# Optimization experiments

Hardware: AMD Instinct MI355X
Metric: run time of the kernel (lower is better)

The kernel has to match this reference:

```python
import jax, jax.numpy as jnp
import numpy as np

N, D, H1, H2, C, K = 8192, 512, 1024, 512, 10, 64
EPS_BN = 1e-5  # torch BatchNorm1d default eps


def _bn(x, g, b):
    # BatchNorm1d in training mode: per-batch stats, biased variance
    mu = x.mean(axis=0)
    var = x.var(axis=0)
    return (x - mu) / jnp.sqrt(var + EPS_BN) * g + b


def _features(x, ibn_g, ibn_b, W1, b1, g1, bb1, W2, b2, g2, bb2):
    x = _bn(x, ibn_g, ibn_b)                    # input_norm
    h = _bn(jnp.tanh(x @ W1.T + b1), g1, bb1)   # layer 1: Linear -> Tanh -> BN
    h = _bn(jnp.tanh(h @ W2.T + b2), g2, bb2)   # layer 2
    return h                                    # [N, H2]


def _nona_self(fx, fn, y_ohe):
    # sim = -cdist(fx, fn); self-neighbor path (x == x_n): -inf diag + top-k mask
    sq_x = jnp.sum(fx * fx, axis=1)
    sq_n = jnp.sum(fn * fn, axis=1)
    d2 = jnp.maximum(sq_x[:, None] + sq_n[None, :] - 2.0 * (fx @ fn.T), 0.0)
    safe = d2 > 1e-9
    dist = jnp.where(safe, jnp.sqrt(jnp.where(safe, d2, 1.0)), 0.0)
    sim = -dist
    eye = jnp.eye(N, dtype=bool)
    sim = jnp.where(eye, -jnp.inf, sim)         # sim -= inf * I
    _, idx = jax.lax.top_k(sim, K)              # [N, K]
    keep = jnp.zeros((N, N), dtype=bool).at[jnp.arange(N)[:, None], idx].set(True)
    sim = jnp.where(keep, sim, -jnp.inf)        # KNNMask: non-topk -> -inf
    probs = jax.nn.softmax(sim, axis=1)
    return jnp.clip(probs @ y_ohe, 0.0, 1.0)


def setup_inputs() -> dict:
    key = jax.random.key(0)
    ks = jax.random.split(key, 6)
    x = jax.random.normal(ks[0], (N, D), dtype=jnp.float32)
    x_n = x + 0.0  # NONA self-neighbor mode requires x_n == x elementwise
    y_n = jax.random.randint(ks[1], (N,), 0, C, dtype=jnp.int32)
    s1 = 1.0 / np.sqrt(D)
    s2 = 1.0 / np.sqrt(H1)
    W1 = jax.random.uniform(ks[2], (H1, D), jnp.float32, -s1, s1)
    b1 = jax.random.uniform(ks[3], (H1,), jnp.float32, -s1, s1)
    W2 = jax.random.uniform(ks[4], (H2, H1), jnp.float32, -s2, s2)
    b2 = jax.random.uniform(ks[5], (H2,), jnp.float32, -s2, s2)
    return {
        "x": x, "x_n": x_n, "y_n": y_n,
        "ibn_g": jnp.ones((D,), jnp.float32), "ibn_b": jnp.zeros((D,), jnp.float32),
        "W1": W1, "b1": b1, "g1": jnp.ones((H1,), jnp.float32), "bb1": jnp.zeros((H1,), jnp.float32),
        "W2": W2, "b2": b2, "g2": jnp.ones((H2,), jnp.float32), "bb2": jnp.zeros((H2,), jnp.float32),
    }


def reference(x, x_n, y_n, ibn_g, ibn_b, W1, b1, g1, bb1, W2, b2, g2, bb2):
    fx = _features(x, ibn_g, ibn_b, W1, b1, g1, bb1, W2, b2, g2, bb2)
    fn = _features(x_n, ibn_g, ibn_b, W1, b1, g1, bb1, W2, b2, g2, bb2)
    y_ohe = jax.nn.one_hot(y_n, C, dtype=jnp.float32)
    return _nona_self(fx, fn, y_ohe)
```

## Files before the change

kernel.cpp:

```cpp
#include <hip/hip_runtime.h>
#include <math.h>

#define NROWS 8192
#define DIM   512
#define HID1  1024
#define HID2  512
#define NCLS  10
#define KTOP  64
#define KPACK 1024
#define KFULL 1536
#define EPSBAND 0.02f

typedef __attribute__((ext_vector_type(8))) short short8;
typedef __attribute__((ext_vector_type(4))) float f32x4;

__device__ __forceinline__ unsigned short f2bf(float x) {
    unsigned u = __float_as_uint(x);
    u += 0x7FFFu + ((u >> 16) & 1u);
    return (unsigned short)(u >> 16);
}
__device__ __forceinline__ float bf2f(unsigned short h) {
    return __uint_as_float(((unsigned)h) << 16);
}

template <typename T>
__global__ __launch_bounds__(256) void col_stats_partial(
    const T* __restrict__ A, int F, int rowsPerBlock,
    double* __restrict__ pSum, double* __restrict__ pSqs)
{
    int c  = blockIdx.x * 256 + threadIdx.x;
    int r0 = blockIdx.y * rowsPerBlock;
    double s = 0.0, s2 = 0.0;
    for (int r = r0; r < r0 + rowsPerBlock; ++r) {
        double v = (double)A[(size_t)r * F + c];
        s  += v;
        s2 += v * v;
    }
    pSum[(size_t)blockIdx.y * F + c] = s;
    pSqs[(size_t)blockIdx.y * F + c] = s2;
}

__global__ __launch_bounds__(256) void col_stats_final(
    const double* __restrict__ pSum, const double* __restrict__ pSqs,
    const float* __restrict__ g, const float* __restrict__ b,
    double* __restrict__ scale, double* __restrict__ shift, int F, int nPart)
{
    int c = blockIdx.x * 256 + threadIdx.x;
    double s = 0.0, s2 = 0.0;
    for (int p = 0; p < nPart; ++p) {
        s  += pSum[(size_t)p * F + c];
        s2 += pSqs[(size_t)p * F + c];
    }
    double mean = s * (1.0 / NROWS);
    double var  = s2 * (1.0 / NROWS) - mean * mean;
    double sc   = (double)g[c] / sqrt(var + 1e-5);
    scale[c] = sc;
    shift[c] = (double)b[c] - mean * sc;
}

template <typename T>
__global__ __launch_bounds__(256) void gemm_affine_tanh(
    const T* __restrict__ A, const double* __restrict__ scl, const double* __restrict__ sft,
    const float* __restrict__ W, const float* __restrict__ bias,
    double* __restrict__ out, int Kd, int F)
{
    __shared__ double aSh[16][68];
    __shared__ double wSh[16][68];
    const int t = threadIdx.x;
    const int fBase = blockIdx.x * 64;
    const int mBase = blockIdx.y * 64;
    const int tm = t & 15, tf = t >> 4;
    const int sm = t >> 2, sk = (t & 3) * 4;
    double acc[4][4] = {};
    for (int k0 = 0; k0 < Kd; k0 += 16) {
        double a0, a1, a2, a3;
        if constexpr (sizeof(T) == 4) {
            float4 av = *(const float4*)&A[(size_t)(mBase + sm) * Kd + k0 + sk];
            a0 = av.x; a1 = av.y; a2 = av.z; a3 = av.w;
        } else {
            const double2* ap = (const double2*)&A[(size_t)(mBase + sm) * Kd + k0 + sk];
            double2 d0 = ap[0], d1 = ap[1];
            a0 = d0.x; a1 = d0.y; a2 = d1.x; a3 = d1.y;
        }
        const double2* sp = (const double2*)&scl[k0 + sk];
        const double2* hp = (const double2*)&sft[k0 + sk];
        double2 s0 = sp[0], s1 = sp[1];
        double2 h0 = hp[0], h1 = hp[1];
        aSh[sk + 0][sm] = a0 * s0.x + h0.x;
        aSh[sk + 1][sm] = a1 * s0.y + h0.y;
        aSh[sk + 2][sm] = a2 * s1.x + h1.x;
        aSh[sk + 3][sm] = a3 * s1.y + h1.y;
        float4 wv = *(const float4*)&W[(size_t)(fBase + sm) * Kd + k0 + sk];
        wSh[sk + 0][sm] = wv.x;
        wSh[sk + 1][sm] = wv.y;
        wSh[sk + 2][sm] = wv.z;
        wSh[sk + 3][sm] = wv.w;
        __syncthreads();
        #pragma unroll
        for (int kk = 0; kk < 16; ++kk) {
            double a4[4], w4[4];
            #pragma unroll
            for (int q = 0; q < 4; ++q) { a4[q] = aSh[kk][tm * 4 + q]; w4[q] = wSh[kk][tf * 4 + q]; }
            #pragma unroll
            for (int i = 0; i < 4; ++i)
                #pragma unroll
                for (int j = 0; j < 4; ++j)
                    acc[i][j] += a4[i] * w4[j];
        }
        __syncthreads();
    }
    #pragma unroll
    for (int i = 0; i < 4; ++i) {
        int m = mBase + tm * 4 + i;
        #pragma unroll
        for (int j = 0; j < 4; ++j) {
            int f = fBase + tf * 4 + j;
            out[(size_t)m * F + f] = tanh(acc[i][j] + (double)bias[f]);
        }
    }
}

__global__ __launch_bounds__(256) void pack_features(
    const double* __restrict__ y2, const double* __restrict__ scl, const double* __restrict__ sft,
    unsigned short* __restrict__ R, float* __restrict__ sqf)
{
    __shared__ double red[4];
    const int r = blockIdx.x;
    const int t = threadIdx.x;
    const int wid = t >> 6, lane = t & 63;
    const int c = t * 2;
    double2 y  = *(const double2*)&y2[(size_t)r * HID2 + c];
    double2 s2 = *(const double2*)&scl[c];
    double2 h2 = *(const double2*)&sft[c];
    double f0 = y.x * s2.x + h2.x;
    double f1 = y.y * s2.y + h2.y;
    unsigned short hi0 = f2bf((float)f0);
    unsigned short hi1 = f2bf((float)f1);
    unsigned short lo0 = f2bf((float)(f0 - (double)bf2f(hi0)));
    unsigned short lo1 = f2bf((float)(f1 - (double)bf2f(hi1)));
    unsigned short* Rr = R + (size_t)r * KPACK;
    Rr[c]           = hi0; Rr[c + 1]           = hi1;
    Rr[HID2 + c]    = lo0; Rr[HID2 + c + 1]    = lo1;
    double s = f0 * f0 + f1 * f1;
    #pragma unroll
    for (int off = 32; off > 0; off >>= 1) s += __shfl_down(s, off);
    if (lane == 0) red[wid] = s;
    __syncthreads();
    if (t == 0) sqf[r] = (float)(red[0] + red[1] + red[2] + red[3]);
}

__global__ __launch_bounds__(256) void sim_mfma(
    const unsigned short* __restrict__ R, const float* __restrict__ sqf,
    float* __restrict__ simbuf, int rowBase)
{
    __shared__ unsigned short aT[128 * 64];
    __shared__ unsigned short bT[128 * 64];
    const int t = threadIdx.x;
    const int wid = t >> 6, lane = t & 63;
    const int wr = wid >> 1, wc = wid & 1;
    const int iBase = rowBase + blockIdx.y * 128;
    const int jBase = blockIdx.x * 128;
    const int srow = lane >> 3;
    const int skk  = (lane & 7) * 8;

    f32x4 zero = {0.f, 0.f, 0.f, 0.f};
    f32x4 acc[4][4];
    #pragma unroll
    for (int m = 0; m < 4; ++m)
        #pragma unroll
        for (int n = 0; n < 4; ++n) acc[m][n] = zero;

    for (int k0 = 0; k0 < KFULL; k0 += 64) {
        const int aSrc = (k0 < 512)  ? k0 : (k0 - 512);
        const int bSrc = (k0 < 1024) ? k0 : (k0 - 1024);
        #pragma unroll
        for (int c = 0; c < 4; ++c) {
            int row = c * 32 + wid * 8 + srow;
            const unsigned short* gpA = R + (size_t)(iBase + row) * KPACK + aSrc + skk;
            const unsigned short* gpB = R + (size_t)(jBase + row) * KPACK + bSrc + skk;
            unsigned short* lpA = &aT[(c * 4 + wid) * 512];
            unsigned short* lpB = &bT[(c * 4 + wid) * 512];
            __builtin_amdgcn_global_load_lds((const __attribute__((address_space(1))) void*)gpA,
                (__attribute__((address_space(3))) void*)lpA, 16, 0, 0);
            __builtin_amdgcn_global_load_lds((const __attribute__((address_space(1))) void*)gpB,
                (__attribute__((address_space(3))) void*)lpB, 16, 0, 0);
        }
        __syncthreads();
        #pragma unroll
        for (int ks = 0; ks < 2; ++ks) {
            short8 aF[4], bF[4];
            #pragma unroll
            for (int m = 0; m < 4; ++m) {
                int rA = wr * 64 + m * 16 + (lane & 15);
                aF[m] = *(const short8*)&aT[rA * 64 + ks * 32 + (lane >> 4) * 8];
            }
            #pragma unroll
            for (int n = 0; n < 4; ++n) {
                int rB = wc * 64 + n * 16 + (lane & 15);
                bF[n] = *(const short8*)&bT[rB * 64 + ks * 32 + (lane >> 4) * 8];
            }
            #pragma unroll
            for (int m = 0; m < 4; ++m)
                #pragma unroll
                for (int n = 0; n < 4; ++n)
                    acc[m][n] = __builtin_amdgcn_mfma_f32_16x16x32_bf16(aF[m], bF[n], acc[m][n], 0, 0, 0);
        }
        __syncthreads();
    }

    #pragma unroll
    for (int m = 0; m < 4; ++m) {
        #pragma unroll
        for (int n = 0; n < 4; ++n) {
            int j = jBase + wc * 64 + n * 16 + (lane & 15);
            float sqj = sqf[j];
            #pragma unroll
            for (int r = 0; r < 4; ++r) {
                int i = iBase + wr * 64 + m * 16 + (lane >> 4) * 4 + r;
                float d2 = sqf[i] + sqj - 2.0f * acc[m][n][r];
                d2 = fmaxf(d2, 0.f);
                float s = (i == j) ? -INFINITY : -d2;
                simbuf[(size_t)(i - rowBase) * NROWS + j] = s;
            }
        }
    }
}

__device__ __forceinline__ unsigned fKey(float v) {
    unsigned b = __float_as_uint(v);
    return (b & 0x80000000u) ? ~b : (b | 0x80000000u);
}
__device__ __forceinline__ float keyToFloat(unsigned k) {
    unsigned b = (k & 0x80000000u) ? (k ^ 0x80000000u) : ~k;
    return __uint_as_float(b);
}

__global__ __launch_bounds__(256) void topk_refine(
    const float* __restrict__ simbuf,
    const double* __restrict__ y2, const double* __restrict__ scl, const double* __restrict__ sft,
    const int* __restrict__ labels, float* __restrict__ out, int rowBase)
{
    __shared__ int      redI[4];
    __shared__ unsigned redU[4];
    __shared__ float    redF[4];
    __shared__ float    cls[NCLS];
    __shared__ int      bandJ[128];
    __shared__ double   bandD2[128];
    __shared__ unsigned char keepB[128];
    __shared__ int      bandCnt;

    const int t = threadIdx.x;
    const int wid = t >> 6, lane = t & 63;
    const int row = blockIdx.x;
    const int gi = rowBase + row;
    const float* srow = simbuf + (size_t)row * NROWS;

    unsigned key[32];
    #pragma unroll
    for (int ii = 0; ii < 32; ++ii) key[ii] = fKey(srow[t + ii * 256]);

    unsigned kmax = 0u;
    #pragma unroll
    for (int ii = 0; ii < 32; ++ii) kmax = max(kmax, key[ii]);
    #pragma unroll
    for (int off = 32; off > 0; off >>= 1) kmax = max(kmax, (unsigned)__shfl_down(kmax, off));
    if (lane == 0) redU[wid] = kmax;
    if (t == 0) bandCnt = 0;
    if (t < NCLS) cls[t] = 0.f;
    __syncthreads();
    kmax = max(max(redU[0], redU[1]), max(redU[2], redU[3]));
    float d2min = fmaxf(-keyToFloat(kmax), 0.f);
    float distMin = (d2min > 1e-9f) ? sqrtf(d2min) : 0.f;
    __syncthreads();

    unsigned lo = 0u, hi = 0xFFFFFFFFu;
    while (lo < hi) {
        unsigned mid = (unsigned)(((unsigned long long)lo + hi + 1ull) >> 1);
        int cnt = 0;
        #pragma unroll
        for (int ii = 0; ii < 32; ++ii) cnt += (key[ii] >= mid) ? 1 : 0;
        #pragma unroll
        for (int off = 32; off > 0; off >>= 1) cnt += __shfl_down(cnt, off);
        if (lane == 0) redI[wid] = cnt;
        __syncthreads();
        int tot = redI[0] + redI[1] + redI[2] + redI[3];
        __syncthreads();
        if (tot >= KTOP) lo = mid; else hi = mid - 1u;
    }
    const float s64 = keyToFloat(lo);
    const unsigned Ku = fKey(s64 + EPSBAND);
    const unsigned Kl = fKey(s64 - EPSBAND);

    int cnt = 0;
    #pragma unroll
    for (int ii = 0; ii < 32; ++ii) cnt += (key[ii] >= Ku) ? 1 : 0;
    #pragma unroll
    for (int off = 32; off > 0; off >>= 1) cnt += __shfl_down(cnt, off);
    if (lane == 0) redI[wid] = cnt;
    __syncthreads();
    const int nSafe = redI[0] + redI[1] + redI[2] + redI[3];
    const int Rslots = KTOP - nSafe;

    #pragma unroll
    for (int ii = 0; ii < 32; ++ii) {
        if (key[ii] >= Kl && key[ii] < Ku) {
            int pos = atomicAdd(&bandCnt, 1);
            if (pos < 128) bandJ[pos] = t + ii * 256;
        }
    }
    __syncthreads();
    const int nb = min(bandCnt, 128);

    for (int c2 = wid; c2 < nb; c2 += 4) {
        int j = bandJ[c2];
        double s = 0.0;
        for (int d = lane; d < HID2; d += 64) {
            double sc = scl[d], sh = sft[d];
            double fi = y2[(size_t)gi * HID2 + d] * sc + sh;
            double fj = y2[(size_t)j  * HID2 + d] * sc + sh;
            double df = fi - fj;
            s += df * df;
        }
        #pragma unroll
        for (int off = 32; off > 0; off >>= 1) s += __shfl_down(s, off);
        if (lane == 0) bandD2[c2] = s;
    }
    __syncthreads();

    for (int c2 = t; c2 < nb; c2 += 256) {
        double d2c = bandD2[c2];
        int jc = bandJ[c2];
        int rank = 0;
        for (int q = 0; q < nb; ++q) {
            double dq = bandD2[q];
            rank += (dq < d2c || (dq == d2c && bandJ[q] < jc)) ? 1 : 0;
        }
        keepB[c2] = (rank < Rslots) ? 1 : 0;
    }
    __syncthreads();

    float S = 0.f;
    #pragma unroll
    for (int ii = 0; ii < 32; ++ii) {
        if (key[ii] >= Ku) {
            float d2 = -keyToFloat(key[ii]);
            float dist = (d2 > 1e-9f) ? sqrtf(d2) : 0.f;
            float w = expf(distMin - dist);
            S += w;
            atomicAdd(&cls[labels[t + ii * 256]], w);
        }
    }
    for (int c2 = t; c2 < nb; c2 += 256) {
        if (keepB[c2]) {
            double dd = bandD2[c2];
            float dist = (dd > 1e-9) ? (float)sqrt(dd) : 0.f;
            float w = expf(distMin - dist);
            S += w;
            atomicAdd(&cls[labels[bandJ[c2]]], w);
        }
    }
    #pragma unroll
    for (int off = 32; off > 0; off >>= 1) S += __shfl_down(S, off);
    if (lane == 0) redF[wid] = S;
    __syncthreads();
    float Stot = redF[0] + redF[1] + redF[2] + redF[3];

    if (t < NCLS) {
        float p = cls[t] / Stot;
        out[(size_t)gi * NCLS + t] = fminf(fmaxf(p, 0.f), 1.f);
    }
}

extern "C" void kernel_launch(void* const* d_in, const int* in_sizes, int n_in,
                              void* d_out, int out_size, void* d_ws, size_t ws_size,
                              hipStream_t stream)
{
    const float* x     = (const float*)d_in[0];
    const int*   y_n   = (const int*)d_in[2];
    const float* ibn_g = (const float*)d_in[3];
    const float* ibn_b = (const float*)d_in[4];
    const float* W1    = (const float*)d_in[5];
    const float* b1    = (const float*)d_in[6];
    const float* g1    = (const float*)d_in[7];
    const float* bb1   = (const float*)d_in[8];
    const float* W2    = (const float*)d_in[9];
    const float* b2    = (const float*)d_in[10];
    const float* g2    = (const float*)d_in[11];
    const float* bb2   = (const float*)d_in[12];
    float* out = (float*)d_out;

    char* ws = (char*)d_ws;
    double*         y1   = (double*)(ws);
    float*          simb = (float*)(ws);
    unsigned short* Rp   = (unsigned short*)(ws + 33554432);
    double*         y2   = (double*)(ws + 67108864);
    double*         pSum = (double*)(ws + 100663296);
    double*         pSqs = (double*)(ws + 101187584);
    double*         prm  = (double*)(ws + 101711872);
    double* scale0 = prm;           double* shift0 = prm + 1024;
    double* scale1 = prm + 2048;    double* shift1 = prm + 3072;
    double* scale2 = prm + 4096;    double* shift2 = prm + 5120;
    float*          sqf  = (float*)(ws + 101761024);

    dim3 blk(256);
    const int RPB = NROWS / 64;

    col_stats_partial<float><<<dim3(DIM / 256, 64), blk, 0, stream>>>(x, DIM, RPB, pSum, pSqs);
    col_stats_final<<<dim3(DIM / 256), blk, 0, stream>>>(pSum, pSqs, ibn_g, ibn_b, scale0, shift0, DIM, 64);
    gemm_affine_tanh<float><<<dim3(HID1 / 64, NROWS / 64), blk, 0, stream>>>(x, scale0, shift0, W1, b1, y1, DIM, HID1);
    col_stats_partial<double><<<dim3(HID1 / 256, 64), blk, 0, stream>>>(y1, HID1, RPB, pSum, pSqs);
    col_stats_final<<<dim3(HID1 / 256), blk, 0, stream>>>(pSum, pSqs, g1, bb1, scale1, shift1, HID1, 64);
    gemm_affine_tanh<double><<<dim3(HID2 / 64, NROWS / 64), blk, 0, stream>>>(y1, scale1, shift1, W2, b2, y2, HID1, HID2);
    col_stats_partial<double><<<dim3(HID2 / 256, 64), blk, 0, stream>>>(y2, HID2, RPB, pSum, pSqs);
    col_stats_final<<<dim3(HID2 / 256), blk, 0, stream>>>(pSum, pSqs, g2, bb2, scale2, shift2, HID2, 64);
    pack_features<<<dim3(NROWS), blk, 0, stream>>>(y2, scale2, shift2, Rp, sqf);
    for (int ch = 0; ch < 8; ++ch) {
        int rowBase = ch * 1024;
        sim_mfma<<<dim3(NROWS / 128, 1024 / 128), blk, 0, stream>>>(Rp, sqf, simb, rowBase);
        topk_refine<<<dim3(1024), blk, 0, stream>>>(simb, y2, scale2, shift2, y_n, out, rowBase);
    }
}
```

Baseline: 1.440 ms.

## Use FP64 MFMA matrix cores for the two feature-layer GEMMs

Replaces the scalar FP64 FMA tiled GEMM with one built on the 16x16x4 FP64 MFMA instruction. Each wave computes a 16x64 output strip. The K chunk grows to 32 and the shared tiles are padded to 66. The aim is to move the double-precision matmul work of both hidden layers from vector ALUs onto matrix cores, which public specs list with higher FP64 throughput. The change also reworks the LDS layout and per-lane fragment indexing, which adds some risk of bank conflicts or fragment mapping errors.

```diff
diff --git a/kernel.cpp b/kernel.cpp
--- a/kernel.cpp
+++ b/kernel.cpp
@@ -13,6 +13,7 @@
 
 typedef __attribute__((ext_vector_type(8))) short short8;
 typedef __attribute__((ext_vector_type(4))) float f32x4;
+typedef __attribute__((ext_vector_type(4))) double f64x4;
 
 __device__ __forceinline__ unsigned short f2bf(float x) {
     unsigned u = __float_as_uint(x);
@@ -59,63 +60,78 @@
 }
 
 template <typename T>
-__global__ __launch_bounds__(256) void gemm_affine_tanh(
+__global__ __launch_bounds__(256) void gemm_mfma_tanh(
     const T* __restrict__ A, const double* __restrict__ scl, const double* __restrict__ sft,
     const float* __restrict__ W, const float* __restrict__ bias,
     double* __restrict__ out, int Kd, int F)
 {
-    __shared__ double aSh[16][68];
-    __shared__ double wSh[16][68];
+    __shared__ double aS[32 * 66];
+    __shared__ double bS[32 * 66];
     const int t = threadIdx.x;
+    const int lane = t & 63;
+    const int wv = t >> 6;
     const int fBase = blockIdx.x * 64;
     const int mBase = blockIdx.y * 64;
-    const int tm = t & 15, tf = t >> 4;
-    const int sm = t >> 2, sk = (t & 3) * 4;
-    double acc[4][4] = {};
-    for (int k0 = 0; k0 < Kd; k0 += 16) {
-        double a0, a1, a2, a3;
+    const int srow = t >> 2;
+    const int skq  = (t & 3) * 8;
+
+    f64x4 acc[4];
+    #pragma unroll
+    for (int n = 0; n < 4; ++n) acc[n] = (f64x4){0.0, 0.0, 0.0, 0.0};
+
+    const int nChunks = Kd >> 5;
+    for (int ch = 0; ch < nChunks; ++ch) {
+        const int kb = ch << 5;
+        double av[8];
         if constexpr (sizeof(T) == 4) {
-            float4 av = *(const float4*)&A[(size_t)(mBase + sm) * Kd + k0 + sk];
-            a0 = av.x; a1 = av.y; a2 = av.z; a3 = av.w;
+            const float4* ap = (const float4*)&A[(size_t)(mBase + srow) * Kd + kb + skq];
+            float4 a0 = ap[0], a1 = ap[1];
+            av[0] = a0.x; av[1] = a0.y; av[2] = a0.z; av[3] = a0.w;
+            av[4] = a1.x; av[5] = a1.y; av[6] = a1.z; av[7] = a1.w;
         } else {
-            const double2* ap = (const double2*)&A[(size_t)(mBase + sm) * Kd + k0 + sk];
-            double2 d0 = ap[0], d1 = ap[1];
-            a0 = d0.x; a1 = d0.y; a2 = d1.x; a3 = d1.y;
-        }
-        const double2* sp = (const double2*)&scl[k0 + sk];
-        const double2* hp = (const double2*)&sft[k0 + sk];
-        double2 s0 = sp[0], s1 = sp[1];
-        double2 h0 = hp[0], h1 = hp[1];
-        aSh[sk + 0][sm] = a0 * s0.x + h0.x;
-        aSh[sk + 1][sm] = a1 * s0.y + h0.y;
-        aSh[sk + 2][sm] = a2 * s1.x + h1.x;
-        aSh[sk + 3][sm] = a3 * s1.y + h1.y;
-        float4 wv = *(const float4*)&W[(size_t)(fBase + sm) * Kd + k0 + sk];
-        wSh[sk + 0][sm] = wv.x;
-        wSh[sk + 1][sm] = wv.y;
-        wSh[sk + 2][sm] = wv.z;
-        wSh[sk + 3][sm] = wv.w;
-        __syncthreads();
-        #pragma unroll
-        for (int kk = 0; kk < 16; ++kk) {
-            double a4[4], w4[4];
+            const double2* ap = (const double2*)&A[(size_t)(mBase + srow) * Kd + kb + skq];
+            double2 d0 = ap[0], d1 = ap[1], d2 = ap[2], d3 = ap[3];
+            av[0] = d0.x; av[1] = d0.y; av[2] = d1.x; av[3] = d1.y;
+            av[4] = d2.x; av[5] = d2.y; av[6] = d3.x; av[7] = d3.y;
+        }
+        #pragma unroll
+        for (int i = 0; i < 8; ++i)
+            av[i] = av[i] * scl[kb + skq + i] + sft[kb + skq + i];
+        #pragma unroll
+        for (int i = 0; i < 8; ++i)
+            aS[(skq + i) * 66 + srow] = av[i];
+        const float4* wp = (const float4*)&W[(size_t)(fBase + srow) * Kd + kb + skq];
+        float4 w0 = wp[0], w1 = wp[1];
+        bS[(skq + 0) * 66 + srow] = (double)w0.x;
+        bS[(skq + 1) * 66 + srow] = (double)w0.y;
+        bS[(skq + 2) * 66 + srow] = (double)w0.z;
+        bS[(skq + 3) * 66 + srow] = (double)w0.w;
+        bS[(skq + 4) * 66 + srow] = (double)w1.x;
+        bS[(skq + 5) * 66 + srow] = (double)w1.y;
+        bS[(skq + 6) * 66 + srow] = (double)w1.z;
+        bS[(skq + 7) * 66 + srow] = (double)w1.w;
+        __syncthreads();
+        #pragma unroll
+        for (int k4 = 0; k4 < 8; ++k4) {
+            const int kk = k4 * 4 + (lane >> 4);
+            double a = aS[kk * 66 + wv * 16 + (lane & 15)];
             #pragma unroll
-            for (int q = 0; q < 4; ++q) { a4[q] = aSh[kk][tm * 4 + q]; w4[q] = wSh[kk][tf * 4 + q]; }
-            #pragma unroll
-            for (int i = 0; i < 4; ++i)
-                #pragma unroll
-                for (int j = 0; j < 4; ++j)
-                    acc[i][j] += a4[i] * w4[j];
-        }
-        __syncthreads();
-    }
-    #pragma unroll
-    for (int i = 0; i < 4; ++i) {
-        int m = mBase + tm * 4 + i;
-        #pragma unroll
-        for (int j = 0; j < 4; ++j) {
-            int f = fBase + tf * 4 + j;
-            out[(size_t)m * F + f] = tanh(acc[i][j] + (double)bias[f]);
+            for (int n = 0; n < 4; ++n) {
+                double b = bS[kk * 66 + n * 16 + (lane & 15)];
+                acc[n] = __builtin_amdgcn_mfma_f64_16x16x4f64(a, b, acc[n], 0, 0, 0);
+            }
+        }
+        __syncthreads();
+    }
+
+    #pragma unroll
+    for (int n = 0; n < 4; ++n) {
+        const int f = fBase + n * 16 + (lane & 15);
+        const double bz = (double)bias[f];
+        #pragma unroll
+        for (int r = 0; r < 4; ++r) {
+            const int m = mBase + wv * 16 + (lane >> 4) * 4 + r;
+            out[(size_t)m * F + f] = tanh(acc[n][r] + bz);
         }
     }
 }
@@ -407,10 +423,10 @@
 
     col_stats_partial<float><<<dim3(DIM / 256, 64), blk, 0, stream>>>(x, DIM, RPB, pSum, pSqs);
     col_stats_final<<<dim3(DIM / 256), blk, 0, stream>>>(pSum, pSqs, ibn_g, ibn_b, scale0, shift0, DIM, 64);
-    gemm_affine_tanh<float><<<dim3(HID1 / 64, NROWS / 64), blk, 0, stream>>>(x, scale0, shift0, W1, b1, y1, DIM, HID1);
+    gemm_mfma_tanh<float><<<dim3(HID1 / 64, NROWS / 64), blk, 0, stream>>>(x, scale0, shift0, W1, b1, y1, DIM, HID1);
     col_stats_partial<double><<<dim3(HID1 / 256, 64), blk, 0, stream>>>(y1, HID1, RPB, pSum, pSqs);
     col_stats_final<<<dim3(HID1 / 256), blk, 0, stream>>>(pSum, pSqs, g1, bb1, scale1, shift1, HID1, 64);
-    gemm_affine_tanh<double><<<dim3(HID2 / 64, NROWS / 64), blk, 0, stream>>>(y1, scale1, shift1, W2, b2, y2, HID1, HID2);
+    gemm_mfma_tanh<double><<<dim3(HID2 / 64, NROWS / 64), blk, 0, stream>>>(y1, scale1, shift1, W2, b2, y2, HID1, HID2);
     col_stats_partial<double><<<dim3(HID2 / 256, 64), blk, 0, stream>>>(y2, HID2, RPB, pSum, pSqs);
     col_stats_final<<<dim3(HID2 / 256), blk, 0, stream>>>(pSum, pSqs, g2, bb2, scale2, shift2, HID2, 64);
     pack_features<<<dim3(NROWS), blk, 0, stream>>>(y2, scale2, shift2, Rp, sqf);
```

New measurement: 1.347 ms. 1.07x faster.
